# Performance work log

Measured on AMD Instinct MI355X. Metric: run time of the kernel, lower is better.

The kernel has to match this reference:

```python
import jax, jax.numpy as jnp
import numpy as np
import math

N, E = 100000, 1600000
IN_FEATS, H, Z_DIM, D, B_COEF = 128, 128, 32, 2, 0.2


def calc_thetas(d):
    # Bernstein-basis thetas, ascending coefficients (matches calculate_theta2)
    thetas = []
    for i in range(d + 1):
        p1 = np.zeros(i + 1); p1[i] = 0.5 ** i               # (x/2)^i
        p2 = np.array([math.comb(d - i, j) * (-0.5) ** j for j in range(d - i + 1)])  # (1-x/2)^(d-i)
        coeffs = np.convolve(p1, p2)                          # length d+1, ascending
        beta = math.gamma(i + 1) * math.gamma(d + 1 - i) / math.gamma(d + 2)
        thetas.append((coeffs / beta).tolist())
    return thetas

THETAS = calc_thetas(D)


def linear(x, w, b):
    return x @ w.T + b


def polyconv(theta, feat, src, dst, d_invsqrt, n):
    h = theta[0] * feat
    for k in range(1, len(theta)):
        tmp = feat * d_invsqrt                                # [N, F]
        agg = jax.ops.segment_sum(tmp[src], dst, num_segments=n)
        feat = feat - agg * d_invsqrt                         # (I - D^-1/2 A D^-1/2) feat
        h = h + theta[k] * feat
    return h


def enc_dec(x, w1, b1, w2, b2, src, dst, d_invsqrt, n):
    x = jax.nn.relu(linear(x, w1, b1))
    hs = jnp.concatenate([polyconv(t, x, src, dst, d_invsqrt, n) for t in THETAS], axis=-1)
    return linear(hs, w2, b2)


def setup_inputs() -> dict:
    key = jax.random.key(0)
    ks = jax.random.split(key, 16)
    nb = len(THETAS)
    return {
        "features": jax.random.normal(ks[0], (N, IN_FEATS), jnp.float32),
        "src": jax.random.randint(ks[1], (E,), 0, N, jnp.int32),
        "dst": jax.random.randint(ks[2], (E,), 0, N, jnp.int32),
        "enc_w1": jax.random.normal(ks[3], (H, IN_FEATS), jnp.float32) * 0.05,
        "enc_b1": jnp.zeros((H,), jnp.float32),
        "enc_w2": jax.random.normal(ks[4], (H, H * nb), jnp.float32) * 0.05,
        "enc_b2": jnp.zeros((H,), jnp.float32),
        "dec_w1": jax.random.normal(ks[5], (IN_FEATS, H), jnp.float32) * 0.05,
        "dec_b1": jnp.zeros((IN_FEATS,), jnp.float32),
        "dec_w2": jax.random.normal(ks[6], (IN_FEATS, IN_FEATS * nb), jnp.float32) * 0.05,
        "dec_b2": jnp.zeros((IN_FEATS,), jnp.float32),
        "rep_w": jax.random.normal(ks[7], (Z_DIM, H), jnp.float32) * 0.05,
        "rep_b": jnp.zeros((Z_DIM,), jnp.float32),
        "rec_w": jax.random.normal(ks[8], (H, Z_DIM), jnp.float32) * 0.05,
        "rec_b": jnp.zeros((H,), jnp.float32),
        "disc_w": jax.random.uniform(ks[9], (H, H), jnp.float32, -1.0 / math.sqrt(H), 1.0 / math.sqrt(H)),
    }


def reference(features, src, dst, enc_w1, enc_b1, enc_w2, enc_b2,
              dec_w1, dec_b1, dec_w2, dec_b2, rep_w, rep_b, rec_w, rec_b, disc_w):
    n = features.shape[0]
    degs = jax.ops.segment_sum(jnp.ones((src.shape[0],), jnp.float32), dst, num_segments=n)
    d_invsqrt = jnp.maximum(degs, 1.0) ** -0.5
    d_invsqrt = d_invsqrt[:, None]

    positive = enc_dec(features, enc_w1, enc_b1, enc_w2, enc_b2, src, dst, d_invsqrt, n)
    perm = jax.random.permutation(jax.random.key(7), n)
    negative = enc_dec(features[perm], enc_w1, enc_b1, enc_w2, enc_b2, src, dst, d_invsqrt, n)

    summary = jax.nn.sigmoid(positive.mean(axis=0))           # [H]
    pos_dis = positive @ (disc_w @ summary)                   # [N]
    neg_dis = negative @ (disc_w @ summary)
    # BCEWithLogits: target=1 -> softplus(-x); target=0 -> softplus(x)
    dgi_loss = jnp.mean(jax.nn.softplus(-pos_dis)) + jnp.mean(jax.nn.softplus(neg_dis))

    mu = linear(positive, rep_w, rep_b)
    log_var = mu
    eps = jax.random.normal(jax.random.key(11), mu.shape, mu.dtype)
    z = mu + eps * jnp.exp(log_var / 2)

    x_rec = enc_dec(linear(z, rec_w, rec_b), dec_w1, dec_b1, dec_w2, dec_b2, src, dst, d_invsqrt, n)
    reconst_loss = jnp.sum((x_rec - features) ** 2)
    kl_div = -0.5 * jnp.sum(1 + log_var - mu ** 2 - jnp.exp(log_var))
    vgae_loss = reconst_loss + kl_div

    ratio = jax.lax.stop_gradient(dgi_loss / vgae_loss)
    return B_COEF * dgi_loss / ratio + (1 - B_COEF) * vgae_loss
```

## Files before the change

kernel.cpp:

```cpp
#include <hip/hip_runtime.h>
#include <math.h>

#define NN   100000
#define EE   1600000
#define F    128
#define ZD   32
#define SCAN_B 256
#define PREP_BLOCKS 161
#define FC1_BLOCKS  1563
#define ENC_BLOCKS  1563
#define NBUCK 391
#define PART_CHUNK 8192
#define PART_BLOCKS 196


typedef float f32x4 __attribute__((ext_vector_type(4)));
typedef int   i32x4 __attribute__((ext_vector_type(4)));
typedef __bf16 bf16x8 __attribute__((ext_vector_type(8)));

__device__ __forceinline__ f32x4 mfma16(i32x4 a, i32x4 b, f32x4 c) {
    return __builtin_amdgcn_mfma_f32_16x16x32_bf16(
        __builtin_bit_cast(bf16x8, a), __builtin_bit_cast(bf16x8, b), c, 0, 0, 0);
}

__device__ __forceinline__ unsigned f2bf(float f) {
    unsigned u = __float_as_uint(f);
    return (u + 0x7fffu + ((u >> 16) & 1u)) >> 16;
}
__device__ __forceinline__ float bf2f(unsigned h) { return __uint_as_float(h << 16); }

__device__ __forceinline__ unsigned pcg_hash(unsigned v) {
    v = v * 747796405u + 2891336453u;
    unsigned w = ((v >> ((v >> 28u) + 4u)) ^ v) * 277803737u;
    return (w >> 22u) ^ w;
}

__device__ __forceinline__ float block_reduce_sum(float v) {
    #pragma unroll
    for (int o = 32; o > 0; o >>= 1) v += __shfl_down(v, o, 64);
    __shared__ float s[8];
    int lane = threadIdx.x & 63, w = threadIdx.x >> 6;
    if (lane == 0) s[w] = v;
    __syncthreads();
    float t = 0.f;
    if (threadIdx.x == 0) {
        int nw = (blockDim.x + 63) >> 6;
        for (int i = 0; i < nw; ++i) t += s[i];
    }
    return t;
}

__global__ __launch_bounds__(256) void prep_deg_kernel(
        const float* __restrict__ repw, const float* __restrict__ w2e,
        const float* __restrict__ b2e,  const float* __restrict__ repb,
        const float* __restrict__ w2d,
        const float* __restrict__ w1d,  const float* __restrict__ recw,
        const float* __restrict__ recb, const float* __restrict__ b1d,
        const float* __restrict__ w1e,
        unsigned short* __restrict__ Wcat,
        float* __restrict__ bmu,
        unsigned short* __restrict__ wd2_a,
        unsigned short* __restrict__ wd2_b,
        unsigned short* __restrict__ wd2_c,
        unsigned short* __restrict__ wrd,
        float* __restrict__ brd,
        unsigned short* __restrict__ w1bf,
        const int* __restrict__ dst, int* __restrict__ degs, int e) {
    int bid = blockIdx.x, tid = threadIdx.x;
    if (bid >= PREP_BLOCKS) {
        int i = (bid - PREP_BLOCKS) * 256 + tid;
        if (i < e) atomicAdd(&degs[dst[i]], 1);
        return;
    }
    if (bid < 16) {
        int idx = bid * 256 + tid;
        int i = idx >> 7, k = idx & 127;
        float m0 = 0.f, m1 = 0.f, m2 = 0.f;
        for (int h = 0; h < 128; ++h) {
            float r = repw[i * 128 + h];
            const float* wr = w2e + (size_t)h * 384 + k;
            m0 += r * wr[0];
            m1 += r * wr[128];
            m2 += r * wr[256];
        }
        Wcat[(size_t)i * 128 + k]        = (unsigned short)f2bf(3.f * m0);
        Wcat[(size_t)(32 + i) * 128 + k] = (unsigned short)f2bf(3.f * (m1 - m0));
        Wcat[(size_t)(64 + i) * 128 + k] = (unsigned short)f2bf(0.75f * m0 - 1.5f * m1 + 0.75f * m2);
    } else if (bid == 16) {
        if (tid < 32) {
            float s = repb[tid];
            for (int h = 0; h < 128; ++h) s += repw[tid * 128 + h] * b2e[h];
            bmu[tid] = s;
        }
    } else if (bid < 81) {
        int idx = (bid - 17) * 256 + tid;
        int j = idx >> 7, k = idx & 127;
        const float* wr = w2d + (size_t)j * 384 + k;
        float w0 = wr[0], w1 = wr[128], w2v = wr[256];
        wd2_a[idx] = (unsigned short)f2bf(3.f * w0);
        wd2_b[idx] = (unsigned short)f2bf(3.f * (w1 - w0));
        wd2_c[idx] = (unsigned short)f2bf(0.75f * w0 - 1.5f * w1 + 0.75f * w2v);
    } else if (bid < 97) {
        int idx = (bid - 81) * 256 + tid;
        int j = idx >> 5, i = idx & 31;
        float s = 0.f;
        for (int h = 0; h < 128; ++h) s += w1d[j * 128 + h] * recw[h * 32 + i];
        wrd[idx] = (unsigned short)f2bf(s);
        if (idx < 128) {
            float b = b1d[idx];
            for (int h = 0; h < 128; ++h) b += w1d[idx * 128 + h] * recb[h];
            brd[idx] = b;
        }
    } else {
        int idx = (bid - 97) * 256 + tid;
        w1bf[idx] = (unsigned short)f2bf(w1e[idx]);
    }
}

__global__ __launch_bounds__(SCAN_B) void scan_block_kernel(const int* __restrict__ degs,
                                                            int* __restrict__ rowstart,
                                                            int* __restrict__ blocksums,
                                                            float* __restrict__ dinv, int n) {
    __shared__ int sh[SCAN_B];
    int i = blockIdx.x * SCAN_B + threadIdx.x;
    int v = (i < n) ? degs[i] : 0;
    sh[threadIdx.x] = v;
    __syncthreads();
    for (int o = 1; o < SCAN_B; o <<= 1) {
        int t = (threadIdx.x >= o) ? sh[threadIdx.x - o] : 0;
        __syncthreads();
        sh[threadIdx.x] += t;
        __syncthreads();
    }
    if (i < n) {
        rowstart[i] = sh[threadIdx.x] - v;
        dinv[i] = 1.f / sqrtf(fmaxf((float)v, 1.f));
    }
    if (threadIdx.x == SCAN_B - 1) blocksums[blockIdx.x] = sh[threadIdx.x];
}

__global__ __launch_bounds__(512) void scan_sums_kernel(int* __restrict__ blocksums, int nb) {
    __shared__ int sh[512];
    int v = (threadIdx.x < nb) ? blocksums[threadIdx.x] : 0;
    sh[threadIdx.x] = v;
    __syncthreads();
    for (int o = 1; o < 512; o <<= 1) {
        int t = (threadIdx.x >= o) ? sh[threadIdx.x - o] : 0;
        __syncthreads();
        sh[threadIdx.x] += t;
        __syncthreads();
    }
    if (threadIdx.x < nb) blocksums[threadIdx.x] = sh[threadIdx.x] - v;
}

__global__ __launch_bounds__(SCAN_B) void scan_add_kernel(int* __restrict__ rowstart,
                                                          int* __restrict__ cursor,
                                                          const int* __restrict__ blocksums,
                                                          int* __restrict__ bstart,
                                                          int* __restrict__ bcursor,
                                                          int n, int e) {
    int i = blockIdx.x * SCAN_B + threadIdx.x;
    if (i < n) {
        int v = rowstart[i] + blocksums[blockIdx.x];
        rowstart[i] = v;
        cursor[i] = v;
        if ((i & 255) == 0) { bstart[i >> 8] = v; bcursor[i >> 8] = v; }
        if (i == 0) bstart[NBUCK] = e;
    }
}

__global__ __launch_bounds__(256) void fc1_part_kernel(const float* __restrict__ x,
                                                       const unsigned short* __restrict__ wbf,
                                                       const float* __restrict__ b,
                                                       unsigned short* __restrict__ out,
                                                       const int* __restrict__ src,
                                                       const int* __restrict__ dst,
                                                       int* __restrict__ bcursor,
                                                       int* __restrict__ ebuf,
                                                       int n, int e) {
    if (blockIdx.x >= FC1_BLOCKS) {
        __shared__ int hist[NBUCK], lofs[NBUCK], gbase[NBUCK];
        int pid = blockIdx.x - FC1_BLOCKS;
        int e0 = pid * PART_CHUNK;
        int e1 = min(e0 + PART_CHUNK, e);
        int tid = threadIdx.x;
        for (int bb = tid; bb < NBUCK; bb += 256) hist[bb] = 0;
        __syncthreads();
        for (int i = e0 + tid; i < e1; i += 256) atomicAdd(&hist[dst[i] >> 8], 1);
        __syncthreads();
        for (int bb = tid; bb < NBUCK; bb += 256) {
            int cct = hist[bb];
            gbase[bb] = cct ? atomicAdd(&bcursor[bb], cct) : 0;
            lofs[bb] = 0;
        }
        __syncthreads();
        for (int i = e0 + tid; i < e1; i += 256) {
            int d = dst[i];
            int bb = d >> 8;
            int pos = gbase[bb] + atomicAdd(&lofs[bb], 1);
            ebuf[pos] = (src[i] << 8) | (d & 255);
        }
        return;
    }
    int wv = threadIdx.x >> 6, lane = threadIdx.x & 63;
    int l16 = lane & 15, lhi = lane >> 4;
    int rowbase = blockIdx.x * 64 + wv * 16;
    int arow = rowbase + l16;
    f32x4 acc[8];
    #pragma unroll
    for (int jt = 0; jt < 8; ++jt) {
        float bj = b[jt * 16 + l16];
        acc[jt] = (f32x4){bj, bj, bj, bj};
    }
    #pragma unroll
    for (int kk = 0; kk < 4; ++kk) {
        int kbase = kk * 32 + lhi * 8;
        i32x4 afrag = {0, 0, 0, 0};
        if (arow < n) {
            const float* ap = x + (size_t)arow * F + kbase;
            f32x4 f0 = *reinterpret_cast<const f32x4*>(ap);
            f32x4 f1 = *reinterpret_cast<const f32x4*>(ap + 4);
            afrag.x = (int)(f2bf(f0.x) | (f2bf(f0.y) << 16));
            afrag.y = (int)(f2bf(f0.z) | (f2bf(f0.w) << 16));
            afrag.z = (int)(f2bf(f1.x) | (f2bf(f1.y) << 16));
            afrag.w = (int)(f2bf(f1.z) | (f2bf(f1.w) << 16));
        }
        #pragma unroll
        for (int jt = 0; jt < 8; ++jt) {
            i32x4 bfrag = *reinterpret_cast<const i32x4*>(wbf + (size_t)(jt * 16 + l16) * F + kbase);
            acc[jt] = mfma16(afrag, bfrag, acc[jt]);
        }
    }
    #pragma unroll
    for (int jt = 0; jt < 8; ++jt)
        #pragma unroll
        for (int r = 0; r < 4; ++r) {
            int row = rowbase + lhi * 4 + r;
            if (row < n)
                out[(size_t)row * F + jt * 16 + l16] =
                    (unsigned short)f2bf(fmaxf(acc[jt][r], 0.f));
        }
}

__global__ __launch_bounds__(256) void encproj_csr_kernel(const unsigned short* __restrict__ A,
                                                          const unsigned short* __restrict__ Wcat,
                                                          unsigned short* __restrict__ G0,
                                                          unsigned short* __restrict__ G1,
                                                          unsigned short* __restrict__ G2,
                                                          const int* __restrict__ ebuf,
                                                          const int* __restrict__ bstart,
                                                          int* __restrict__ cursor,
                                                          int* __restrict__ csr_src,
                                                          int n) {
    if (blockIdx.x >= ENC_BLOCKS) {
        int bb = blockIdx.x - ENC_BLOCKS;
        int s0 = bstart[bb], s1 = bstart[bb + 1];
        for (int i = s0 + (int)threadIdx.x; i < s1; i += 256) {
            int p = ebuf[i];
            int d = (bb << 8) | (p & 255);
            int pos = atomicAdd(&cursor[d], 1);
            csr_src[pos] = p >> 8;
        }
        return;
    }
    int wv = threadIdx.x >> 6, lane = threadIdx.x & 63;
    int l16 = lane & 15, lhi = lane >> 4;
    int rowbase = blockIdx.x * 64 + wv * 16;
    int arow = rowbase + l16;
    f32x4 acc[6];
    #pragma unroll
    for (int jt = 0; jt < 6; ++jt) acc[jt] = (f32x4){0.f, 0.f, 0.f, 0.f};
    #pragma unroll
    for (int kk = 0; kk < 4; ++kk) {
        int kbase = kk * 32 + lhi * 8;
        i32x4 afrag = {0, 0, 0, 0};
        if (arow < n)
            afrag = *reinterpret_cast<const i32x4*>(A + (size_t)arow * F + kbase);
        #pragma unroll
        for (int jt = 0; jt < 6; ++jt) {
            i32x4 bfrag = *reinterpret_cast<const i32x4*>(Wcat + (size_t)(jt * 16 + l16) * F + kbase);
            acc[jt] = mfma16(afrag, bfrag, acc[jt]);
        }
    }
    #pragma unroll
    for (int jt = 0; jt < 6; ++jt)
        #pragma unroll
        for (int r = 0; r < 4; ++r) {
            int row = rowbase + lhi * 4 + r;
            int j = jt * 16 + l16;
            if (row < n) {
                unsigned short v = (unsigned short)f2bf(acc[jt][r]);
                if (j < 32)      G0[(size_t)row * 32 + j] = v;
                else if (j < 64) G1[(size_t)row * 32 + (j - 32)] = v;
                else             G2[(size_t)row * 32 + (j - 64)] = v;
            }
        }
}

__global__ __launch_bounds__(256) void gather32_W_kernel(const unsigned short* __restrict__ G2,
                                                         const unsigned short* __restrict__ G1,
                                                         const int* __restrict__ csr_src,
                                                         const int* __restrict__ rowstart,
                                                         const int* __restrict__ degs,
                                                         const float* __restrict__ dinv,
                                                         unsigned short* __restrict__ W, int n) {
    int r = blockIdx.x * 16 + (threadIdx.x >> 4);
    if (r >= n) return;
    int lane = threadIdx.x & 15;
    int c = lane * 2;
    int start = rowstart[r], deg = degs[r];
    float ax = 0.f, ay = 0.f;
    for (int base = 0; base < deg; base += 16) {
        int cnt = min(deg - base, 16);
        int s = 0; float sc = 0.f;
        if (lane < cnt) { s = csr_src[start + base + lane]; sc = dinv[s]; }
        int k = 0;
        for (; k + 4 <= cnt; k += 4) {
            int s0 = __shfl(s, k, 16), s1 = __shfl(s, k + 1, 16);
            int s2 = __shfl(s, k + 2, 16), s3 = __shfl(s, k + 3, 16);
            float c0 = __shfl(sc, k, 16), c1 = __shfl(sc, k + 1, 16);
            float c2 = __shfl(sc, k + 2, 16), c3 = __shfl(sc, k + 3, 16);
            unsigned v0 = *reinterpret_cast<const unsigned*>(G2 + (size_t)s0 * 32 + c);
            unsigned v1 = *reinterpret_cast<const unsigned*>(G2 + (size_t)s1 * 32 + c);
            unsigned v2 = *reinterpret_cast<const unsigned*>(G2 + (size_t)s2 * 32 + c);
            unsigned v3 = *reinterpret_cast<const unsigned*>(G2 + (size_t)s3 * 32 + c);
            ax += bf2f(v0 & 0xffffu) * c0 + bf2f(v1 & 0xffffu) * c1
                + bf2f(v2 & 0xffffu) * c2 + bf2f(v3 & 0xffffu) * c3;
            ay += bf2f(v0 >> 16) * c0 + bf2f(v1 >> 16) * c1
                + bf2f(v2 >> 16) * c2 + bf2f(v3 >> 16) * c3;
        }
        for (; k < cnt; ++k) {
            int sk = __shfl(s, k, 16);
            float ck = __shfl(sc, k, 16);
            unsigned v = *reinterpret_cast<const unsigned*>(G2 + (size_t)sk * 32 + c);
            ax += bf2f(v & 0xffffu) * ck;
            ay += bf2f(v >> 16) * ck;
        }
    }
    float di = dinv[r];
    unsigned g2v = *reinterpret_cast<const unsigned*>(G2 + (size_t)r * 32 + c);
    unsigned g1v = *reinterpret_cast<const unsigned*>(G1 + (size_t)r * 32 + c);
    float wx = bf2f(g1v & 0xffffu) + bf2f(g2v & 0xffffu) - di * ax;
    float wy = bf2f(g1v >> 16)     + bf2f(g2v >> 16)     - di * ay;
    *reinterpret_cast<unsigned*>(W + (size_t)r * 32 + c) = f2bf(wx) | (f2bf(wy) << 16);
}

__global__ __launch_bounds__(256) void gather32_mukl_kernel(const unsigned short* __restrict__ W,
                                                            const unsigned short* __restrict__ G0,
                                                            const int* __restrict__ csr_src,
                                                            const int* __restrict__ rowstart,
                                                            const int* __restrict__ degs,
                                                            const float* __restrict__ dinv,
                                                            const float* __restrict__ bmu,
                                                            unsigned short* __restrict__ Z,
                                                            double* __restrict__ accd, int n) {
    int r = blockIdx.x * 16 + (threadIdx.x >> 4);
    int lane = threadIdx.x & 15;
    int c = lane * 2;
    float kl = 0.f;
    if (r < n) {
        int start = rowstart[r], deg = degs[r];
        float ax = 0.f, ay = 0.f;
        for (int base = 0; base < deg; base += 16) {
            int cnt = min(deg - base, 16);
            int s = 0; float sc = 0.f;
            if (lane < cnt) { s = csr_src[start + base + lane]; sc = dinv[s]; }
            int k = 0;
            for (; k + 4 <= cnt; k += 4) {
                int s0 = __shfl(s, k, 16), s1 = __shfl(s, k + 1, 16);
                int s2 = __shfl(s, k + 2, 16), s3 = __shfl(s, k + 3, 16);
                float c0 = __shfl(sc, k, 16), c1 = __shfl(sc, k + 1, 16);
                float c2 = __shfl(sc, k + 2, 16), c3 = __shfl(sc, k + 3, 16);
                unsigned v0 = *reinterpret_cast<const unsigned*>(W + (size_t)s0 * 32 + c);
                unsigned v1 = *reinterpret_cast<const unsigned*>(W + (size_t)s1 * 32 + c);
                unsigned v2 = *reinterpret_cast<const unsigned*>(W + (size_t)s2 * 32 + c);
                unsigned v3 = *reinterpret_cast<const unsigned*>(W + (size_t)s3 * 32 + c);
                ax += bf2f(v0 & 0xffffu) * c0 + bf2f(v1 & 0xffffu) * c1
                    + bf2f(v2 & 0xffffu) * c2 + bf2f(v3 & 0xffffu) * c3;
                ay += bf2f(v0 >> 16) * c0 + bf2f(v1 >> 16) * c1
                    + bf2f(v2 >> 16) * c2 + bf2f(v3 >> 16) * c3;
            }
            for (; k < cnt; ++k) {
                int sk = __shfl(s, k, 16);
                float ck = __shfl(sc, k, 16);
                unsigned v = *reinterpret_cast<const unsigned*>(W + (size_t)sk * 32 + c);
                ax += bf2f(v & 0xffffu) * ck;
                ay += bf2f(v >> 16) * ck;
            }
        }
        float di = dinv[r];
        unsigned wv = *reinterpret_cast<const unsigned*>(W + (size_t)r * 32 + c);
        unsigned g0v = *reinterpret_cast<const unsigned*>(G0 + (size_t)r * 32 + c);
        float mu0 = bf2f(g0v & 0xffffu) + bf2f(wv & 0xffffu) - di * ax + bmu[c];
        float mu1 = bf2f(g0v >> 16)     + bf2f(wv >> 16)     - di * ay + bmu[c + 1];
        kl = (1.f + mu0 - mu0 * mu0 - expf(mu0)) + (1.f + mu1 - mu1 * mu1 - expf(mu1));
        unsigned idx0 = (unsigned)(r * ZD + c);
        unsigned h1 = pcg_hash(2u * idx0 + 1u);
        unsigned h2 = pcg_hash(2u * idx0 + 2u);
        float u1 = ((float)h1 + 0.5f) * 2.3283064365386963e-10f;
        float u2 = ((float)h2 + 0.5f) * 2.3283064365386963e-10f;
        float eps0 = sqrtf(-2.f * logf(u1)) * cosf(6.283185307179586f * u2);
        unsigned idx1 = idx0 + 1u;
        unsigned h3 = pcg_hash(2u * idx1 + 1u);
        unsigned h4 = pcg_hash(2u * idx1 + 2u);
        float u3 = ((float)h3 + 0.5f) * 2.3283064365386963e-10f;
        float u4 = ((float)h4 + 0.5f) * 2.3283064365386963e-10f;
        float eps1 = sqrtf(-2.f * logf(u3)) * cosf(6.283185307179586f * u4);
        float z0 = mu0 + eps0 * expf(0.5f * mu0);
        float z1 = mu1 + eps1 * expf(0.5f * mu1);
        *reinterpret_cast<unsigned*>(Z + (size_t)r * ZD + c) = f2bf(z0) | (f2bf(z1) << 16);
    }
    float bs = block_reduce_sum(kl);
    if (threadIdx.x == 0) atomicAdd(&accd[1], (double)bs);
}

__global__ __launch_bounds__(256) void gather128_kernel(const unsigned short* __restrict__ x,
                                                        const int* __restrict__ csr_src,
                                                        const int* __restrict__ rowstart,
                                                        const int* __restrict__ degs,
                                                        const float* __restrict__ dinv,
                                                        unsigned short* __restrict__ out, int n) {
    int r = blockIdx.x * 4 + (threadIdx.x >> 6);
    if (r >= n) return;
    int lane = threadIdx.x & 63;
    int c = lane * 2;
    int start = rowstart[r], deg = degs[r];
    float ax = 0.f, ay = 0.f;
    for (int base = 0; base < deg; base += 64) {
        int cnt = min(deg - base, 64);
        int s = 0; float sc = 0.f;
        if (lane < cnt) { s = csr_src[start + base + lane]; sc = dinv[s]; }
        int k = 0;
        for (; k + 4 <= cnt; k += 4) {
            int s0 = __shfl(s, k), s1 = __shfl(s, k + 1);
            int s2 = __shfl(s, k + 2), s3 = __shfl(s, k + 3);
            float c0 = __shfl(sc, k), c1 = __shfl(sc, k + 1);
            float c2 = __shfl(sc, k + 2), c3 = __shfl(sc, k + 3);
            unsigned v0 = *reinterpret_cast<const unsigned*>(x + (size_t)s0 * F + c);
            unsigned v1 = *reinterpret_cast<const unsigned*>(x + (size_t)s1 * F + c);
            unsigned v2 = *reinterpret_cast<const unsigned*>(x + (size_t)s2 * F + c);
            unsigned v3 = *reinterpret_cast<const unsigned*>(x + (size_t)s3 * F + c);
            ax += bf2f(v0 & 0xffffu) * c0 + bf2f(v1 & 0xffffu) * c1
                + bf2f(v2 & 0xffffu) * c2 + bf2f(v3 & 0xffffu) * c3;
            ay += bf2f(v0 >> 16) * c0 + bf2f(v1 >> 16) * c1
                + bf2f(v2 >> 16) * c2 + bf2f(v3 >> 16) * c3;
        }
        for (; k < cnt; ++k) {
            int sk = __shfl(s, k);
            float ck = __shfl(sc, k);
            unsigned v = *reinterpret_cast<const unsigned*>(x + (size_t)sk * F + c);
            ax += bf2f(v & 0xffffu) * ck;
            ay += bf2f(v >> 16) * ck;
        }
    }
    float di = dinv[r];
    unsigned xv = *reinterpret_cast<const unsigned*>(x + (size_t)r * F + c);
    float ox = bf2f(xv & 0xffffu) - di * ax;
    float oy = bf2f(xv >> 16) - di * ay;
    *reinterpret_cast<unsigned*>(out + (size_t)r * F + c) = f2bf(ox) | (f2bf(oy) << 16);
}

__global__ __launch_bounds__(256) void recdec1_mfma_kernel(const unsigned short* __restrict__ Z,
                                                           const unsigned short* __restrict__ Wrd,
                                                           const float* __restrict__ brd,
                                                           unsigned short* __restrict__ out, int n) {
    int wv = threadIdx.x >> 6, lane = threadIdx.x & 63;
    int l16 = lane & 15, lhi = lane >> 4;
    int rowbase = blockIdx.x * 64 + wv * 16;
    int arow = rowbase + l16;
    int kbase = lhi * 8;
    i32x4 afrag = {0, 0, 0, 0};
    if (arow < n)
        afrag = *reinterpret_cast<const i32x4*>(Z + (size_t)arow * ZD + kbase);
    #pragma unroll
    for (int jt = 0; jt < 8; ++jt) {
        float bj = brd[jt * 16 + l16];
        f32x4 acc = (f32x4){bj, bj, bj, bj};
        i32x4 bfrag = *reinterpret_cast<const i32x4*>(Wrd + (size_t)(jt * 16 + l16) * ZD + kbase);
        acc = mfma16(afrag, bfrag, acc);
        #pragma unroll
        for (int r = 0; r < 4; ++r) {
            int row = rowbase + lhi * 4 + r;
            if (row < n)
                out[(size_t)row * F + jt * 16 + l16] =
                    (unsigned short)f2bf(fmaxf(acc[r], 0.f));
        }
    }
}

__global__ __launch_bounds__(256) void dec2loss_mfma_kernel(const unsigned short* __restrict__ A,
                                                            const unsigned short* __restrict__ B,
                                                            const unsigned short* __restrict__ C,
                                                            const unsigned short* __restrict__ Wa,
                                                            const unsigned short* __restrict__ Wb,
                                                            const unsigned short* __restrict__ Wc,
                                                            const float* __restrict__ b2,
                                                            const float* __restrict__ feats,
                                                            double* __restrict__ accd, int n) {
    __shared__ __align__(16) unsigned short wsh[128 * 128];
    int tid = threadIdx.x;
    int wv = tid >> 6, lane = tid & 63;
    int l16 = lane & 15, lhi = lane >> 4;
    int rowbase = blockIdx.x * 64 + wv * 16;
    int arow = rowbase + l16;
    float fpre[8][4];
    #pragma unroll
    for (int jt = 0; jt < 8; ++jt)
        #pragma unroll
        for (int r = 0; r < 4; ++r) {
            int row = rowbase + lhi * 4 + r;
            fpre[jt][r] = (row < n) ? feats[(size_t)row * F + jt * 16 + l16] : 0.f;
        }
    f32x4 acc[8];
    #pragma unroll
    for (int jt = 0; jt < 8; ++jt) {
        float bj = b2[jt * 16 + l16];
        acc[jt] = (f32x4){bj, bj, bj, bj};
    }
    const unsigned short* mats[3] = {A, B, C};
    const unsigned short* wsrc[3] = {Wa, Wb, Wc};
    #pragma unroll
    for (int s = 0; s < 3; ++s) {
        __syncthreads();
        #pragma unroll
        for (int it = 0; it < 8; ++it) {
            int idx = it * 256 + tid;
            int j = idx >> 4;
            int colb = (idx & 15) << 4;
            i32x4 v = *reinterpret_cast<const i32x4*>(wsrc[s] + (size_t)j * 128 + ((idx & 15) << 3));
            *reinterpret_cast<i32x4*>((char*)wsh + j * 256 + (colb ^ ((j & 7) << 4))) = v;
        }
        __syncthreads();
        #pragma unroll
        for (int kk = 0; kk < 4; ++kk) {
            i32x4 afrag = {0, 0, 0, 0};
            if (arow < n)
                afrag = *reinterpret_cast<const i32x4*>(mats[s] + (size_t)arow * F + kk * 32 + lhi * 8);
            #pragma unroll
            for (int jt = 0; jt < 8; ++jt) {
                int j = jt * 16 + l16;
                int colb = (kk * 64 + lhi * 16) ^ ((j & 7) << 4);
                i32x4 bfrag = *reinterpret_cast<const i32x4*>((const char*)wsh + j * 256 + colb);
                acc[jt] = mfma16(afrag, bfrag, acc[jt]);
            }
        }
    }
    float local = 0.f;
    #pragma unroll
    for (int jt = 0; jt < 8; ++jt)
        #pragma unroll
        for (int r = 0; r < 4; ++r) {
            int row = rowbase + lhi * 4 + r;
            if (row < n) {
                float d = acc[jt][r] - fpre[jt][r];
                local += d * d;
            }
        }
    float bs = block_reduce_sum(local);
    if (threadIdx.x == 0) atomicAdd(&accd[0], (double)bs);
}

__global__ void finalize_kernel(const double* __restrict__ acc, float* __restrict__ out) {
    out[0] = (float)(acc[0] - 0.5 * acc[1]);
}

extern "C" void kernel_launch(void* const* d_in, const int* in_sizes, int n_in,
                              void* d_out, int out_size, void* d_ws, size_t ws_size,
                              hipStream_t stream) {
    const float* feats  = (const float*)d_in[0];
    const int*   src    = (const int*)d_in[1];
    const int*   dst    = (const int*)d_in[2];
    const float* enc_w1 = (const float*)d_in[3];
    const float* enc_b1 = (const float*)d_in[4];
    const float* enc_w2 = (const float*)d_in[5];
    const float* enc_b2 = (const float*)d_in[6];
    const float* dec_w1 = (const float*)d_in[7];
    const float* dec_b1 = (const float*)d_in[8];
    const float* dec_w2 = (const float*)d_in[9];
    const float* dec_b2 = (const float*)d_in[10];
    const float* rep_w  = (const float*)d_in[11];
    const float* rep_b  = (const float*)d_in[12];
    const float* rec_w  = (const float*)d_in[13];
    const float* rec_b  = (const float*)d_in[14];

    const int n = NN, e = EE;
    char* ws = (char*)d_ws;
    size_t off = 0;
    auto alloc = [&](size_t bytes) -> void* {
        void* p = ws + off;
        off += (bytes + 255) & ~(size_t)255;
        return p;
    };
    const size_t NFB = (size_t)n * F * sizeof(unsigned short);
    const int nScanBlocks = (n + SCAN_B - 1) / SCAN_B;
    int*    degs    = (int*)alloc((size_t)n * sizeof(int));
    float*  dinv    = (float*)alloc((size_t)n * sizeof(float));
    int*    rowst   = (int*)alloc((size_t)n * sizeof(int));
    int*    cursor  = (int*)alloc((size_t)n * sizeof(int));
    int*    bsums   = (int*)alloc((size_t)nScanBlocks * sizeof(int));
    int*    bstart  = (int*)alloc((NBUCK + 1) * sizeof(int));
    int*    bcursor = (int*)alloc(NBUCK * sizeof(int));
    int*    ebuf    = (int*)alloc((size_t)e * sizeof(int));
    int*    csr_src = (int*)alloc((size_t)e * sizeof(int));
    unsigned short* Abf = (unsigned short*)alloc(NFB);
    unsigned short* Bbf = (unsigned short*)alloc(NFB);
    unsigned short* Cbf = (unsigned short*)alloc(NFB);
    unsigned short* G0  = (unsigned short*)alloc((size_t)n * 32 * sizeof(unsigned short));
    unsigned short* G1  = (unsigned short*)alloc((size_t)n * 32 * sizeof(unsigned short));
    unsigned short* G2  = (unsigned short*)alloc((size_t)n * 32 * sizeof(unsigned short));
    unsigned short* Wg  = (unsigned short*)alloc((size_t)n * 32 * sizeof(unsigned short));
    unsigned short* Zbf = (unsigned short*)alloc((size_t)n * ZD * sizeof(unsigned short));
    unsigned short* Wcat  = (unsigned short*)alloc(96 * 128 * sizeof(unsigned short));
    unsigned short* w1bf  = (unsigned short*)alloc(128 * 128 * sizeof(unsigned short));
    unsigned short* wd2_a = (unsigned short*)alloc(128 * 128 * sizeof(unsigned short));
    unsigned short* wd2_b = (unsigned short*)alloc(128 * 128 * sizeof(unsigned short));
    unsigned short* wd2_c = (unsigned short*)alloc(128 * 128 * sizeof(unsigned short));
    unsigned short* wrd   = (unsigned short*)alloc(128 * 32 * sizeof(unsigned short));
    float* bmu = (float*)alloc(32 * sizeof(float));
    float* brd = (float*)alloc(128 * sizeof(float));
    double* acc = (double*)alloc(2 * sizeof(double));

    const int gemm64   = (n + 63) / 64;
    const int csrBlks  = (e + 255) / 256;
    const int gathBlks = (n + 3) / 4;
    const int g32Blks  = (n + 15) / 16;

    hipMemsetAsync(degs, 0, (size_t)n * sizeof(int), stream);
    hipMemsetAsync(acc, 0, 2 * sizeof(double), stream);

    prep_deg_kernel<<<PREP_BLOCKS + csrBlks, 256, 0, stream>>>(
        rep_w, enc_w2, enc_b2, rep_b, dec_w2, dec_w1, rec_w, rec_b, dec_b1, enc_w1,
        Wcat, bmu, wd2_a, wd2_b, wd2_c, wrd, brd, w1bf, dst, degs, e);

    scan_block_kernel<<<nScanBlocks, SCAN_B, 0, stream>>>(degs, rowst, bsums, dinv, n);
    scan_sums_kernel<<<1, 512, 0, stream>>>(bsums, nScanBlocks);
    scan_add_kernel<<<nScanBlocks, SCAN_B, 0, stream>>>(rowst, cursor, bsums,
                                                        bstart, bcursor, n, e);

    fc1_part_kernel<<<FC1_BLOCKS + PART_BLOCKS, 256, 0, stream>>>(
        feats, w1bf, enc_b1, Abf, src, dst, bcursor, ebuf, n, e);

    encproj_csr_kernel<<<ENC_BLOCKS + NBUCK, 256, 0, stream>>>(
        Abf, Wcat, G0, G1, G2, ebuf, bstart, cursor, csr_src, n);

    gather32_W_kernel<<<g32Blks, 256, 0, stream>>>(G2, G1, csr_src, rowst, degs, dinv, Wg, n);
    gather32_mukl_kernel<<<g32Blks, 256, 0, stream>>>(Wg, G0, csr_src, rowst, degs, dinv,
                                                      bmu, Zbf, acc, n);

    recdec1_mfma_kernel<<<gemm64, 256, 0, stream>>>(Zbf, wrd, brd, Abf, n);
    gather128_kernel<<<gathBlks, 256, 0, stream>>>(Abf, csr_src, rowst, degs, dinv, Bbf, n);
    gather128_kernel<<<gathBlks, 256, 0, stream>>>(Bbf, csr_src, rowst, degs, dinv, Cbf, n);
    dec2loss_mfma_kernel<<<gemm64, 256, 0, stream>>>(Abf, Bbf, Cbf, wd2_a, wd2_b, wd2_c,
                                                     dec_b2, feats, acc, n);

    finalize_kernel<<<1, 1, 0, stream>>>(acc, (float*)d_out);
}
```

Measured before the change: 502.5 us.

## Store features pre-scaled by D^-1/2 to drop per-edge dinv gathers

Node features stored for propagation are now pre-multiplied by dinv (in the encoder projection and decoder first layer), so the gather kernels sum raw neighbor rows and apply dinv^2 once per node instead of loading dinv[src] for every edge. A sqrt(deg) array is added to undo the scaling where the unscaled value is needed (mu computation, decoder loss with bias moved out). The gather inner loops are also unrolled to 8 independent loads. This removes a random per-edge gather and its shuffles, but scaled values now go through bf16 storage in a different form, which can shift rounding error.

```diff
diff --git a/kernel.cpp b/kernel.cpp
--- a/kernel.cpp
+++ b/kernel.cpp
@@ -120,7 +120,8 @@
 __global__ __launch_bounds__(SCAN_B) void scan_block_kernel(const int* __restrict__ degs,
                                                             int* __restrict__ rowstart,
                                                             int* __restrict__ blocksums,
-                                                            float* __restrict__ dinv, int n) {
+                                                            float* __restrict__ dinv,
+                                                            float* __restrict__ rsq, int n) {
     __shared__ int sh[SCAN_B];
     int i = blockIdx.x * SCAN_B + threadIdx.x;
     int v = (i < n) ? degs[i] : 0;
@@ -134,7 +135,10 @@
     }
     if (i < n) {
         rowstart[i] = sh[threadIdx.x] - v;
-        dinv[i] = 1.f / sqrtf(fmaxf((float)v, 1.f));
+        float d = fmaxf((float)v, 1.f);
+        float s = sqrtf(d);
+        rsq[i] = s;
+        dinv[i] = 1.f / s;
     }
     if (threadIdx.x == SCAN_B - 1) blocksums[blockIdx.x] = sh[threadIdx.x];
 }
@@ -244,9 +248,10 @@
 
 __global__ __launch_bounds__(256) void encproj_csr_kernel(const unsigned short* __restrict__ A,
                                                           const unsigned short* __restrict__ Wcat,
+                                                          const float* __restrict__ dinv,
                                                           unsigned short* __restrict__ G0,
-                                                          unsigned short* __restrict__ G1,
-                                                          unsigned short* __restrict__ G2,
+                                                          unsigned short* __restrict__ G1s,
+                                                          unsigned short* __restrict__ G2s,
                                                           const int* __restrict__ ebuf,
                                                           const int* __restrict__ bstart,
                                                           int* __restrict__ cursor,
@@ -267,6 +272,12 @@
     int l16 = lane & 15, lhi = lane >> 4;
     int rowbase = blockIdx.x * 64 + wv * 16;
     int arow = rowbase + l16;
+    float dv[4];
+    #pragma unroll
+    for (int r = 0; r < 4; ++r) {
+        int row = rowbase + lhi * 4 + r;
+        dv[r] = (row < n) ? dinv[row] : 1.f;
+    }
     f32x4 acc[6];
     #pragma unroll
     for (int jt = 0; jt < 6; ++jt) acc[jt] = (f32x4){0.f, 0.f, 0.f, 0.f};
@@ -289,16 +300,19 @@
             int row = rowbase + lhi * 4 + r;
             int j = jt * 16 + l16;
             if (row < n) {
-                unsigned short v = (unsigned short)f2bf(acc[jt][r]);
-                if (j < 32)      G0[(size_t)row * 32 + j] = v;
-                else if (j < 64) G1[(size_t)row * 32 + (j - 32)] = v;
-                else             G2[(size_t)row * 32 + (j - 64)] = v;
-            }
-        }
-}
-
-__global__ __launch_bounds__(256) void gather32_W_kernel(const unsigned short* __restrict__ G2,
-                                                         const unsigned short* __restrict__ G1,
+                if (j < 32) {
+                    G0[(size_t)row * 32 + j] = (unsigned short)f2bf(acc[jt][r]);
+                } else if (j < 64) {
+                    G1s[(size_t)row * 32 + (j - 32)] = (unsigned short)f2bf(acc[jt][r] * dv[r]);
+                } else {
+                    G2s[(size_t)row * 32 + (j - 64)] = (unsigned short)f2bf(acc[jt][r] * dv[r]);
+                }
+            }
+        }
+}
+
+__global__ __launch_bounds__(256) void gather32_W_kernel(const unsigned short* __restrict__ G2s,
+                                                         const unsigned short* __restrict__ G1s,
                                                          const int* __restrict__ csr_src,
                                                          const int* __restrict__ rowstart,
                                                          const int* __restrict__ degs,
@@ -312,36 +326,35 @@
     float ax = 0.f, ay = 0.f;
     for (int base = 0; base < deg; base += 16) {
         int cnt = min(deg - base, 16);
-        int s = 0; float sc = 0.f;
-        if (lane < cnt) { s = csr_src[start + base + lane]; sc = dinv[s]; }
+        int s = 0;
+        if (lane < cnt) s = csr_src[start + base + lane];
         int k = 0;
-        for (; k + 4 <= cnt; k += 4) {
-            int s0 = __shfl(s, k, 16), s1 = __shfl(s, k + 1, 16);
-            int s2 = __shfl(s, k + 2, 16), s3 = __shfl(s, k + 3, 16);
-            float c0 = __shfl(sc, k, 16), c1 = __shfl(sc, k + 1, 16);
-            float c2 = __shfl(sc, k + 2, 16), c3 = __shfl(sc, k + 3, 16);
-            unsigned v0 = *reinterpret_cast<const unsigned*>(G2 + (size_t)s0 * 32 + c);
-            unsigned v1 = *reinterpret_cast<const unsigned*>(G2 + (size_t)s1 * 32 + c);
-            unsigned v2 = *reinterpret_cast<const unsigned*>(G2 + (size_t)s2 * 32 + c);
-            unsigned v3 = *reinterpret_cast<const unsigned*>(G2 + (size_t)s3 * 32 + c);
-            ax += bf2f(v0 & 0xffffu) * c0 + bf2f(v1 & 0xffffu) * c1
-                + bf2f(v2 & 0xffffu) * c2 + bf2f(v3 & 0xffffu) * c3;
-            ay += bf2f(v0 >> 16) * c0 + bf2f(v1 >> 16) * c1
-                + bf2f(v2 >> 16) * c2 + bf2f(v3 >> 16) * c3;
+        for (; k + 8 <= cnt; k += 8) {
+            unsigned v[8];
+            #pragma unroll
+            for (int q = 0; q < 8; ++q) {
+                int sq = __shfl(s, k + q, 16);
+                v[q] = *reinterpret_cast<const unsigned*>(G2s + (size_t)sq * 32 + c);
+            }
+            #pragma unroll
+            for (int q = 0; q < 8; ++q) {
+                ax += bf2f(v[q] & 0xffffu);
+                ay += bf2f(v[q] >> 16);
+            }
         }
         for (; k < cnt; ++k) {
             int sk = __shfl(s, k, 16);
-            float ck = __shfl(sc, k, 16);
-            unsigned v = *reinterpret_cast<const unsigned*>(G2 + (size_t)sk * 32 + c);
-            ax += bf2f(v & 0xffffu) * ck;
-            ay += bf2f(v >> 16) * ck;
+            unsigned v = *reinterpret_cast<const unsigned*>(G2s + (size_t)sk * 32 + c);
+            ax += bf2f(v & 0xffffu);
+            ay += bf2f(v >> 16);
         }
     }
     float di = dinv[r];
-    unsigned g2v = *reinterpret_cast<const unsigned*>(G2 + (size_t)r * 32 + c);
-    unsigned g1v = *reinterpret_cast<const unsigned*>(G1 + (size_t)r * 32 + c);
-    float wx = bf2f(g1v & 0xffffu) + bf2f(g2v & 0xffffu) - di * ax;
-    float wy = bf2f(g1v >> 16)     + bf2f(g2v >> 16)     - di * ay;
+    float di2 = di * di;
+    unsigned g2v = *reinterpret_cast<const unsigned*>(G2s + (size_t)r * 32 + c);
+    unsigned g1v = *reinterpret_cast<const unsigned*>(G1s + (size_t)r * 32 + c);
+    float wx = bf2f(g1v & 0xffffu) + bf2f(g2v & 0xffffu) - di2 * ax;
+    float wy = bf2f(g1v >> 16)     + bf2f(g2v >> 16)     - di2 * ay;
     *reinterpret_cast<unsigned*>(W + (size_t)r * 32 + c) = f2bf(wx) | (f2bf(wy) << 16);
 }
 
@@ -351,6 +364,7 @@
                                                             const int* __restrict__ rowstart,
                                                             const int* __restrict__ degs,
                                                             const float* __restrict__ dinv,
+                                                            const float* __restrict__ rsq,
                                                             const float* __restrict__ bmu,
                                                             unsigned short* __restrict__ Z,
                                                             double* __restrict__ accd, int n) {
@@ -363,36 +377,35 @@
         float ax = 0.f, ay = 0.f;
         for (int base = 0; base < deg; base += 16) {
             int cnt = min(deg - base, 16);
-            int s = 0; float sc = 0.f;
-            if (lane < cnt) { s = csr_src[start + base + lane]; sc = dinv[s]; }
+            int s = 0;
+            if (lane < cnt) s = csr_src[start + base + lane];
             int k = 0;
-            for (; k + 4 <= cnt; k += 4) {
-                int s0 = __shfl(s, k, 16), s1 = __shfl(s, k + 1, 16);
-                int s2 = __shfl(s, k + 2, 16), s3 = __shfl(s, k + 3, 16);
-                float c0 = __shfl(sc, k, 16), c1 = __shfl(sc, k + 1, 16);
-                float c2 = __shfl(sc, k + 2, 16), c3 = __shfl(sc, k + 3, 16);
-                unsigned v0 = *reinterpret_cast<const unsigned*>(W + (size_t)s0 * 32 + c);
-                unsigned v1 = *reinterpret_cast<const unsigned*>(W + (size_t)s1 * 32 + c);
-                unsigned v2 = *reinterpret_cast<const unsigned*>(W + (size_t)s2 * 32 + c);
-                unsigned v3 = *reinterpret_cast<const unsigned*>(W + (size_t)s3 * 32 + c);
-                ax += bf2f(v0 & 0xffffu) * c0 + bf2f(v1 & 0xffffu) * c1
-                    + bf2f(v2 & 0xffffu) * c2 + bf2f(v3 & 0xffffu) * c3;
-                ay += bf2f(v0 >> 16) * c0 + bf2f(v1 >> 16) * c1
-                    + bf2f(v2 >> 16) * c2 + bf2f(v3 >> 16) * c3;
+            for (; k + 8 <= cnt; k += 8) {
+                unsigned v[8];
+                #pragma unroll
+                for (int q = 0; q < 8; ++q) {
+                    int sq = __shfl(s, k + q, 16);
+                    v[q] = *reinterpret_cast<const unsigned*>(W + (size_t)sq * 32 + c);
+                }
+                #pragma unroll
+                for (int q = 0; q < 8; ++q) {
+                    ax += bf2f(v[q] & 0xffffu);
+                    ay += bf2f(v[q] >> 16);
+                }
             }
             for (; k < cnt; ++k) {
                 int sk = __shfl(s, k, 16);
-                float ck = __shfl(sc, k, 16);
                 unsigned v = *reinterpret_cast<const unsigned*>(W + (size_t)sk * 32 + c);
-                ax += bf2f(v & 0xffffu) * ck;
-                ay += bf2f(v >> 16) * ck;
+                ax += bf2f(v & 0xffffu);
+                ay += bf2f(v >> 16);
             }
         }
         float di = dinv[r];
+        float rs = rsq[r];
         unsigned wv = *reinterpret_cast<const unsigned*>(W + (size_t)r * 32 + c);
         unsigned g0v = *reinterpret_cast<const unsigned*>(G0 + (size_t)r * 32 + c);
-        float mu0 = bf2f(g0v & 0xffffu) + bf2f(wv & 0xffffu) - di * ax + bmu[c];
-        float mu1 = bf2f(g0v >> 16)     + bf2f(wv >> 16)     - di * ay + bmu[c + 1];
+        float mu0 = bf2f(g0v & 0xffffu) + rs * bf2f(wv & 0xffffu) - di * ax + bmu[c];
+        float mu1 = bf2f(g0v >> 16)     + rs * bf2f(wv >> 16)     - di * ay + bmu[c + 1];
         kl = (1.f + mu0 - mu0 * mu0 - expf(mu0)) + (1.f + mu1 - mu1 * mu1 - expf(mu1));
         unsigned idx0 = (unsigned)(r * ZD + c);
         unsigned h1 = pcg_hash(2u * idx0 + 1u);
@@ -428,47 +441,53 @@
     float ax = 0.f, ay = 0.f;
     for (int base = 0; base < deg; base += 64) {
         int cnt = min(deg - base, 64);
-        int s = 0; float sc = 0.f;
-        if (lane < cnt) { s = csr_src[start + base + lane]; sc = dinv[s]; }
+        int s = 0;
+        if (lane < cnt) s = csr_src[start + base + lane];
         int k = 0;
-        for (; k + 4 <= cnt; k += 4) {
-            int s0 = __shfl(s, k), s1 = __shfl(s, k + 1);
-            int s2 = __shfl(s, k + 2), s3 = __shfl(s, k + 3);
-            float c0 = __shfl(sc, k), c1 = __shfl(sc, k + 1);
-            float c2 = __shfl(sc, k + 2), c3 = __shfl(sc, k + 3);
-            unsigned v0 = *reinterpret_cast<const unsigned*>(x + (size_t)s0 * F + c);
-            unsigned v1 = *reinterpret_cast<const unsigned*>(x + (size_t)s1 * F + c);
-            unsigned v2 = *reinterpret_cast<const unsigned*>(x + (size_t)s2 * F + c);
-            unsigned v3 = *reinterpret_cast<const unsigned*>(x + (size_t)s3 * F + c);
-            ax += bf2f(v0 & 0xffffu) * c0 + bf2f(v1 & 0xffffu) * c1
-                + bf2f(v2 & 0xffffu) * c2 + bf2f(v3 & 0xffffu) * c3;
-            ay += bf2f(v0 >> 16) * c0 + bf2f(v1 >> 16) * c1
-                + bf2f(v2 >> 16) * c2 + bf2f(v3 >> 16) * c3;
+        for (; k + 8 <= cnt; k += 8) {
+            unsigned v[8];
+            #pragma unroll
+            for (int q = 0; q < 8; ++q) {
+                int sq = __shfl(s, k + q);
+                v[q] = *reinterpret_cast<const unsigned*>(x + (size_t)sq * F + c);
+            }
+            #pragma unroll
+            for (int q = 0; q < 8; ++q) {
+                ax += bf2f(v[q] & 0xffffu);
+                ay += bf2f(v[q] >> 16);
+            }
         }
         for (; k < cnt; ++k) {
             int sk = __shfl(s, k);
-            float ck = __shfl(sc, k);
             unsigned v = *reinterpret_cast<const unsigned*>(x + (size_t)sk * F + c);
-            ax += bf2f(v & 0xffffu) * ck;
-            ay += bf2f(v >> 16) * ck;
+            ax += bf2f(v & 0xffffu);
+            ay += bf2f(v >> 16);
         }
     }
     float di = dinv[r];
+    float di2 = di * di;
     unsigned xv = *reinterpret_cast<const unsigned*>(x + (size_t)r * F + c);
-    float ox = bf2f(xv & 0xffffu) - di * ax;
-    float oy = bf2f(xv >> 16) - di * ay;
+    float ox = bf2f(xv & 0xffffu) - di2 * ax;
+    float oy = bf2f(xv >> 16) - di2 * ay;
     *reinterpret_cast<unsigned*>(out + (size_t)r * F + c) = f2bf(ox) | (f2bf(oy) << 16);
 }
 
 __global__ __launch_bounds__(256) void recdec1_mfma_kernel(const unsigned short* __restrict__ Z,
                                                            const unsigned short* __restrict__ Wrd,
                                                            const float* __restrict__ brd,
+                                                           const float* __restrict__ dinv,
                                                            unsigned short* __restrict__ out, int n) {
     int wv = threadIdx.x >> 6, lane = threadIdx.x & 63;
     int l16 = lane & 15, lhi = lane >> 4;
     int rowbase = blockIdx.x * 64 + wv * 16;
     int arow = rowbase + l16;
     int kbase = lhi * 8;
+    float dv[4];
+    #pragma unroll
+    for (int r = 0; r < 4; ++r) {
+        int row = rowbase + lhi * 4 + r;
+        dv[r] = (row < n) ? dinv[row] : 1.f;
+    }
     i32x4 afrag = {0, 0, 0, 0};
     if (arow < n)
         afrag = *reinterpret_cast<const i32x4*>(Z + (size_t)arow * ZD + kbase);
@@ -483,7 +502,7 @@
             int row = rowbase + lhi * 4 + r;
             if (row < n)
                 out[(size_t)row * F + jt * 16 + l16] =
-                    (unsigned short)f2bf(fmaxf(acc[r], 0.f));
+                    (unsigned short)f2bf(fmaxf(acc[r], 0.f) * dv[r]);
         }
     }
 }
@@ -495,6 +514,7 @@
                                                             const unsigned short* __restrict__ Wb,
                                                             const unsigned short* __restrict__ Wc,
                                                             const float* __restrict__ b2,
+                                                            const float* __restrict__ rsq,
                                                             const float* __restrict__ feats,
                                                             double* __restrict__ accd, int n) {
     __shared__ __align__(16) unsigned short wsh[128 * 128];
@@ -504,6 +524,12 @@
     int rowbase = blockIdx.x * 64 + wv * 16;
     int arow = rowbase + l16;
     float fpre[8][4];
+    float rsv[4];
+    #pragma unroll
+    for (int r = 0; r < 4; ++r) {
+        int row = rowbase + lhi * 4 + r;
+        rsv[r] = (row < n) ? rsq[row] : 1.f;
+    }
     #pragma unroll
     for (int jt = 0; jt < 8; ++jt)
         #pragma unroll
@@ -513,10 +539,7 @@
         }
     f32x4 acc[8];
     #pragma unroll
-    for (int jt = 0; jt < 8; ++jt) {
-        float bj = b2[jt * 16 + l16];
-        acc[jt] = (f32x4){bj, bj, bj, bj};
-    }
+    for (int jt = 0; jt < 8; ++jt) acc[jt] = (f32x4){0.f, 0.f, 0.f, 0.f};
     const unsigned short* mats[3] = {A, B, C};
     const unsigned short* wsrc[3] = {Wa, Wb, Wc};
     #pragma unroll
@@ -547,15 +570,17 @@
     }
     float local = 0.f;
     #pragma unroll
-    for (int jt = 0; jt < 8; ++jt)
+    for (int jt = 0; jt < 8; ++jt) {
+        float bj = b2[jt * 16 + l16];
         #pragma unroll
         for (int r = 0; r < 4; ++r) {
             int row = rowbase + lhi * 4 + r;
             if (row < n) {
-                float d = acc[jt][r] - fpre[jt][r];
+                float d = acc[jt][r] * rsv[r] + bj - fpre[jt][r];
                 local += d * d;
             }
         }
+    }
     float bs = block_reduce_sum(local);
     if (threadIdx.x == 0) atomicAdd(&accd[0], (double)bs);
 }
@@ -595,6 +620,7 @@
     const int nScanBlocks = (n + SCAN_B - 1) / SCAN_B;
     int*    degs    = (int*)alloc((size_t)n * sizeof(int));
     float*  dinv    = (float*)alloc((size_t)n * sizeof(float));
+    float*  rsq     = (float*)alloc((size_t)n * sizeof(float));
     int*    rowst   = (int*)alloc((size_t)n * sizeof(int));
     int*    cursor  = (int*)alloc((size_t)n * sizeof(int));
     int*    bsums   = (int*)alloc((size_t)nScanBlocks * sizeof(int));
@@ -632,7 +658,7 @@
         rep_w, enc_w2, enc_b2, rep_b, dec_w2, dec_w1, rec_w, rec_b, dec_b1, enc_w1,
         Wcat, bmu, wd2_a, wd2_b, wd2_c, wrd, brd, w1bf, dst, degs, e);
 
-    scan_block_kernel<<<nScanBlocks, SCAN_B, 0, stream>>>(degs, rowst, bsums, dinv, n);
+    scan_block_kernel<<<nScanBlocks, SCAN_B, 0, stream>>>(degs, rowst, bsums, dinv, rsq, n);
     scan_sums_kernel<<<1, 512, 0, stream>>>(bsums, nScanBlocks);
     scan_add_kernel<<<nScanBlocks, SCAN_B, 0, stream>>>(rowst, cursor, bsums,
                                                         bstart, bcursor, n, e);
@@ -641,17 +667,17 @@
         feats, w1bf, enc_b1, Abf, src, dst, bcursor, ebuf, n, e);
 
     encproj_csr_kernel<<<ENC_BLOCKS + NBUCK, 256, 0, stream>>>(
-        Abf, Wcat, G0, G1, G2, ebuf, bstart, cursor, csr_src, n);
+        Abf, Wcat, dinv, G0, G1, G2, ebuf, bstart, cursor, csr_src, n);
 
     gather32_W_kernel<<<g32Blks, 256, 0, stream>>>(G2, G1, csr_src, rowst, degs, dinv, Wg, n);
     gather32_mukl_kernel<<<g32Blks, 256, 0, stream>>>(Wg, G0, csr_src, rowst, degs, dinv,
-                                                      bmu, Zbf, acc, n);
-
-    recdec1_mfma_kernel<<<gemm64, 256, 0, stream>>>(Zbf, wrd, brd, Abf, n);
+                                                      rsq, bmu, Zbf, acc, n);
+
+    recdec1_mfma_kernel<<<gemm64, 256, 0, stream>>>(Zbf, wrd, brd, dinv, Abf, n);
     gather128_kernel<<<gathBlks, 256, 0, stream>>>(Abf, csr_src, rowst, degs, dinv, Bbf, n);
     gather128_kernel<<<gathBlks, 256, 0, stream>>>(Bbf, csr_src, rowst, degs, dinv, Cbf, n);
     dec2loss_mfma_kernel<<<gemm64, 256, 0, stream>>>(Abf, Bbf, Cbf, wd2_a, wd2_b, wd2_c,
-                                                     dec_b2, feats, acc, n);
+                                                     dec_b2, rsq, feats, acc, n);
 
     finalize_kernel<<<1, 1, 0, stream>>>(acc, (float*)d_out);
 }
```

New measurement: 501.4 us. About the same (-0.2%).
